# Kernel optimization log

Measured on AMD Instinct MI355X. Metric: run time of the kernel, lower is better.

Reference implementation:

```python
import jax, jax.numpy as jnp
import numpy as np

VOCAB, BLOCK, L, D, H, HD, K = 32000, 4096, 4, 512, 8, 64, 256
EPS = float(jnp.finfo(jnp.float32).eps)


def setup_inputs() -> dict:
    key = jax.random.key(0)
    ks = jax.random.split(key, 16)
    s = 0.02
    inp = {
        "tokens": jax.random.randint(ks[0], (2, 4096), 0, VOCAB),
        "E": jax.random.normal(ks[1], (VOCAB, D), jnp.float32) * s,   # tied token emb / lm_head
        "P": jax.random.normal(ks[2], (BLOCK, D), jnp.float32) * s,   # pos emb
        "Wr": jax.random.normal(ks[3], (L, H, D), jnp.float32) * s,   # router
        "Wq": jax.random.normal(ks[4], (L, D, D), jnp.float32) * s,
        "Wk": jax.random.normal(ks[5], (L, D, D), jnp.float32) * s,
        "Wv": jax.random.normal(ks[6], (L, D, D), jnp.float32) * s,
        "Wo": jax.random.normal(ks[7], (L, D, D), jnp.float32) * s,
        "n1": jnp.ones((L, D), jnp.float32),   # RMSNorm weights
        "n2": jnp.ones((L, D), jnp.float32),
        "W1": jax.random.normal(ks[8], (L, 4 * D, D), jnp.float32) * s,
        "b1": jnp.zeros((L, 4 * D), jnp.float32),
        "W2": jax.random.normal(ks[9], (L, D, 4 * D), jnp.float32) * s,
        "b2": jnp.zeros((L, D), jnp.float32),
    }
    return inp


def rmsnorm(x, w):
    return x * jax.lax.rsqrt(jnp.mean(x * x, axis=-1, keepdims=True) + EPS) * w


def subq_attention(x, Wr, Wq, Wk, Wv, Wo):
    B, T, _ = x.shape
    k_eff = min(K, T)
    # per-head router scores [B, H, T] -> top-k token indices per head
    r = jnp.einsum('btd,hd->bht', x, Wr)
    _, idx = jax.lax.top_k(r, k_eff)                     # [B, H, k]
    q = (x @ Wq.T).reshape(B, T, H, HD).transpose(0, 2, 1, 3)  # [B,H,T,hd]
    k = (x @ Wk.T).reshape(B, T, H, HD).transpose(0, 2, 1, 3)
    v = (x @ Wv.T).reshape(B, T, H, HD).transpose(0, 2, 1, 3)
    ig = idx[..., None]                                   # [B,H,k,1]
    qg = jnp.take_along_axis(q, ig, axis=2)               # [B,H,k,hd]
    kg = jnp.take_along_axis(k, ig, axis=2)
    vg = jnp.take_along_axis(v, ig, axis=2)
    scale = HD ** -0.5
    s = jnp.einsum('bhkd,bhjd->bhkj', qg, kg) * scale     # [B,H,k,k]
    can_attend = idx[:, :, :, None] >= idx[:, :, None, :]  # causal in ORIGINAL positions
    s = jnp.where(can_attend, s, -jnp.inf)
    a = jax.nn.softmax(s, axis=-1)
    og = jnp.einsum('bhkj,bhjd->bhkd', a, vg)             # [B,H,k,hd]
    bb = jnp.arange(B)[:, None, None]
    hh = jnp.arange(H)[None, :, None]
    out = jnp.zeros((B, H, T, HD), x.dtype).at[bb, hh, idx].set(og)  # scatter (indices unique)
    out = out.transpose(0, 2, 1, 3).reshape(B, T, D)
    return out @ Wo.T


def gpt_forward(tokens, E, P, Wr, Wq, Wk, Wv, Wo, n1, n2, W1, b1, W2, b2):
    T = tokens.shape[1]
    x = E[tokens] + P[:T][None, :, :]
    for l in range(L):
        x = x + subq_attention(rmsnorm(x, n1[l]), Wr[l], Wq[l], Wk[l], Wv[l], Wo[l])
        h = rmsnorm(x, n2[l])
        x = x + (jax.nn.silu(h @ W1[l].T + b1[l]) @ W2[l].T + b2[l])
    return x @ E.T  # tied lm_head


def reference(tokens, E, P, Wr, Wq, Wk, Wv, Wo, n1, n2, W1, b1, W2, b2):
    return gpt_forward(tokens, E, P, Wr, Wq, Wk, Wv, Wo, n1, n2, W1, b1, W2, b2)
```

## Files before the change

kernel.cpp:

```cpp
#include <hip/hip_runtime.h>
#include <math.h>

#define BB   2
#define TT   4096
#define DD   512
#define HH   8
#define HDD  64
#define KK   256
#define FF   2048
#define VV   32000
#define LL   4
#define EPSF 1.1920928955078125e-07f

__global__ void embed_k(const int* __restrict__ tok, const float* __restrict__ E,
                        const float* __restrict__ P, float* __restrict__ X) {
    int idx = blockIdx.x * blockDim.x + threadIdx.x;
    int d  = idx & (DD - 1);
    int bt = idx / DD;
    int t  = bt & (TT - 1);
    X[idx] = E[(size_t)tok[bt] * DD + d] + P[t * DD + d];
}

__global__ void rmsnorm_k(const float* __restrict__ X, const float* __restrict__ w,
                          float* __restrict__ Hout) {
    int row = blockIdx.x;
    const float* x = X + (size_t)row * DD;
    int tid = threadIdx.x;
    float v0 = x[tid], v1 = x[tid + 256];
    float ss = v0 * v0 + v1 * v1;
    for (int off = 32; off; off >>= 1) ss += __shfl_down(ss, off);
    __shared__ float red[4];
    __shared__ float sfac;
    if ((tid & 63) == 0) red[tid >> 6] = ss;
    __syncthreads();
    if (tid == 0) {
        float s = red[0] + red[1] + red[2] + red[3];
        sfac = rsqrtf(s * (1.0f / DD) + EPSF);
    }
    __syncthreads();
    float f = sfac;
    Hout[(size_t)row * DD + tid]       = v0 * f * w[tid];
    Hout[(size_t)row * DD + tid + 256] = v1 * f * w[tid + 256];
}

__global__ void router_k(const float* __restrict__ Hb, const float* __restrict__ Wr,
                         float* __restrict__ R) {
    int t = blockIdx.x, h = blockIdx.y, b = blockIdx.z;
    int lane = threadIdx.x;
    const float* x = Hb + ((size_t)(b * TT + t)) * DD;
    const float* w = Wr + h * DD;
    float s = 0.f;
    for (int c = lane; c < DD; c += 64) s += x[c] * w[c];
    for (int off = 32; off; off >>= 1) s += __shfl_down(s, off);
    if (lane == 0) R[((size_t)(b * HH + h)) * TT + t] = s;
}

__global__ void select_k(const float* __restrict__ R, int* __restrict__ IDX) {
    int h = blockIdx.y, b = blockIdx.z;
    const float* r = R + ((size_t)(b * HH + h)) * TT;
    __shared__ float sr[TT];
    for (int i = threadIdx.x; i < TT; i += 256) sr[i] = r[i];
    __syncthreads();
    int t = blockIdx.x * 256 + threadIdx.x;
    float v = sr[t];
    int rank = 0;
    for (int u = 0; u < TT; u++) {
        float ru = sr[u];
        rank += (ru > v) || (ru == v && u < t);
    }
    if (rank < KK) IDX[(b * HH + h) * KK + rank] = t;
}

__global__ void qkv_k(const float* __restrict__ Hb, const int* __restrict__ IDX,
                      const float* __restrict__ Wq, const float* __restrict__ Wk,
                      const float* __restrict__ Wv,
                      float* __restrict__ QG, float* __restrict__ KG, float* __restrict__ VG) {
    int i = blockIdx.x, h = blockIdx.y, b = blockIdx.z;
    int bh = b * HH + h;
    int ti = IDX[bh * KK + i];
    __shared__ float xr[DD];
    int tid = threadIdx.x;
    for (int c = tid; c < DD; c += 192) xr[c] = Hb[((size_t)(b * TT + ti)) * DD + c];
    __syncthreads();
    int which = tid / 64, d = tid & 63;
    const float* W = (which == 0) ? Wq : (which == 1) ? Wk : Wv;
    const float* wrow = W + (size_t)(h * HDD + d) * DD;
    float s = 0.f;
    for (int c = 0; c < DD; c++) s += xr[c] * wrow[c];
    float* Out = (which == 0) ? QG : (which == 1) ? KG : VG;
    Out[((size_t)(bh * KK + i)) * HDD + d] = s;
}

__global__ void attn_k(const float* __restrict__ QG, const float* __restrict__ KG,
                       const float* __restrict__ VG, const int* __restrict__ IDX,
                       float* __restrict__ OG) {
    int i = blockIdx.x, h = blockIdx.y, b = blockIdx.z;
    int bh = b * HH + h;
    const int* idx = IDX + bh * KK;
    __shared__ float q[HDD];
    __shared__ float a[KK];
    __shared__ float red[4];
    int tid = threadIdx.x;
    int ti = idx[i];
    if (tid < HDD) q[tid] = QG[((size_t)(bh * KK + i)) * HDD + tid];
    __syncthreads();
    int j = tid;
    const float* krow = KG + ((size_t)(bh * KK + j)) * HDD;
    float s = 0.f;
    for (int c = 0; c < HDD; c++) s += q[c] * krow[c];
    int tj = idx[j];
    s = (ti >= tj) ? s * 0.125f : -INFINITY;
    float m = s;
    for (int off = 32; off; off >>= 1) m = fmaxf(m, __shfl_down(m, off));
    if ((tid & 63) == 0) red[tid >> 6] = m;
    __syncthreads();
    if (tid == 0) red[0] = fmaxf(fmaxf(red[0], red[1]), fmaxf(red[2], red[3]));
    __syncthreads();
    float mall = red[0];
    float e = expf(s - mall);
    float sum = e;
    for (int off = 32; off; off >>= 1) sum += __shfl_down(sum, off);
    __syncthreads();
    if ((tid & 63) == 0) red[tid >> 6] = sum;
    __syncthreads();
    if (tid == 0) red[0] = red[0] + red[1] + red[2] + red[3];
    __syncthreads();
    float denom = red[0];
    a[tid] = e / denom;
    __syncthreads();
    if (tid < HDD) {
        float o = 0.f;
        for (int jj = 0; jj < KK; jj++) o += a[jj] * VG[((size_t)(bh * KK + jj)) * HDD + tid];
        OG[((size_t)(bh * KK + i)) * HDD + tid] = o;
    }
}

__global__ void oproj_k(const float* __restrict__ OG, const int* __restrict__ IDX,
                        const float* __restrict__ Wo, float* __restrict__ X) {
    int i = blockIdx.x, h = blockIdx.y, b = blockIdx.z;
    int bh = b * HH + h;
    __shared__ float og[HDD];
    int tid = threadIdx.x;
    if (tid < HDD) og[tid] = OG[((size_t)(bh * KK + i)) * HDD + tid];
    __syncthreads();
    int ti = IDX[bh * KK + i];
    const float* wr = Wo + (size_t)tid * DD + h * HDD;
    float s = 0.f;
    for (int c = 0; c < HDD; c++) s += og[c] * wr[c];
    atomicAdd(&X[((size_t)(b * TT + ti)) * DD + tid], s);
}

template <int ACT, int ACC>
__global__ __launch_bounds__(256) void gemm_bt_k(const float* __restrict__ A,
                                                 const float* __restrict__ B,
                                                 const float* __restrict__ bias,
                                                 float* __restrict__ C,
                                                 int M, int N, int Kd) {
    __shared__ float As[16][65];
    __shared__ float Bs[16][65];
    int tx = threadIdx.x, ty = threadIdx.y;
    int tid = ty * 16 + tx;
    int n0 = blockIdx.x * 64, m0 = blockIdx.y * 64;
    float c[4][4] = {};
    int lrow = tid >> 4;
    int lcol = tid & 15;
    for (int k0 = 0; k0 < Kd; k0 += 16) {
#pragma unroll
        for (int i = 0; i < 4; i++) {
            int row = lrow + i * 16;
            As[lcol][row] = A[(size_t)(m0 + row) * Kd + k0 + lcol];
            Bs[lcol][row] = B[(size_t)(n0 + row) * Kd + k0 + lcol];
        }
        __syncthreads();
#pragma unroll
        for (int kk = 0; kk < 16; kk++) {
            float a0 = As[kk][ty * 4 + 0], a1 = As[kk][ty * 4 + 1];
            float a2 = As[kk][ty * 4 + 2], a3 = As[kk][ty * 4 + 3];
            float b0 = Bs[kk][tx * 4 + 0], b1 = Bs[kk][tx * 4 + 1];
            float b2 = Bs[kk][tx * 4 + 2], b3 = Bs[kk][tx * 4 + 3];
            c[0][0] += a0 * b0; c[0][1] += a0 * b1; c[0][2] += a0 * b2; c[0][3] += a0 * b3;
            c[1][0] += a1 * b0; c[1][1] += a1 * b1; c[1][2] += a1 * b2; c[1][3] += a1 * b3;
            c[2][0] += a2 * b0; c[2][1] += a2 * b1; c[2][2] += a2 * b2; c[2][3] += a2 * b3;
            c[3][0] += a3 * b0; c[3][1] += a3 * b1; c[3][2] += a3 * b2; c[3][3] += a3 * b3;
        }
        __syncthreads();
    }
#pragma unroll
    for (int i = 0; i < 4; i++) {
#pragma unroll
        for (int j = 0; j < 4; j++) {
            int m = m0 + ty * 4 + i;
            int n = n0 + tx * 4 + j;
            float v = c[i][j];
            if (bias) v += bias[n];
            if (ACT == 1) v = v / (1.0f + expf(-v));
            size_t o = (size_t)m * N + n;
            if (ACC) C[o] += v; else C[o] = v;
        }
    }
}

extern "C" void kernel_launch(void* const* d_in, const int* in_sizes, int n_in,
                              void* d_out, int out_size, void* d_ws, size_t ws_size,
                              hipStream_t stream) {
    const int*   tok = (const int*)d_in[0];
    const float* E   = (const float*)d_in[1];
    const float* P   = (const float*)d_in[2];
    const float* Wr  = (const float*)d_in[3];
    const float* Wq  = (const float*)d_in[4];
    const float* Wk  = (const float*)d_in[5];
    const float* Wv  = (const float*)d_in[6];
    const float* Wo  = (const float*)d_in[7];
    const float* n1  = (const float*)d_in[8];
    const float* n2  = (const float*)d_in[9];
    const float* W1  = (const float*)d_in[10];
    const float* b1  = (const float*)d_in[11];
    const float* W2  = (const float*)d_in[12];
    const float* b2  = (const float*)d_in[13];
    float* OUT = (float*)d_out;

    float* X = (float*)d_ws;
    float* U   = OUT;
    float* Hb  = U + (size_t)8192 * FF;
    float* R   = Hb + (size_t)8192 * DD;
    float* QG  = R + BB * HH * TT;
    float* KG  = QG + BB * HH * KK * HDD;
    float* VG  = KG + BB * HH * KK * HDD;
    float* OG  = VG + BB * HH * KK * HDD;
    int*   IDX = (int*)(OG + BB * HH * KK * HDD);

    embed_k<<<BB * TT * DD / 256, 256, 0, stream>>>(tok, E, P, X);

    for (int l = 0; l < LL; l++) {
        const float* Wql = Wq + (size_t)l * DD * DD;
        const float* Wkl = Wk + (size_t)l * DD * DD;
        const float* Wvl = Wv + (size_t)l * DD * DD;
        const float* Wol = Wo + (size_t)l * DD * DD;

        rmsnorm_k<<<BB * TT, 256, 0, stream>>>(X, n1 + l * DD, Hb);
        router_k<<<dim3(TT, HH, BB), 64, 0, stream>>>(Hb, Wr + l * HH * DD, R);
        select_k<<<dim3(TT / 256, HH, BB), 256, 0, stream>>>(R, IDX);
        qkv_k<<<dim3(KK, HH, BB), 192, 0, stream>>>(Hb, IDX, Wql, Wkl, Wvl, QG, KG, VG);
        attn_k<<<dim3(KK, HH, BB), 256, 0, stream>>>(QG, KG, VG, IDX, OG);
        oproj_k<<<dim3(KK, HH, BB), 512, 0, stream>>>(OG, IDX, Wol, X);

        rmsnorm_k<<<BB * TT, 256, 0, stream>>>(X, n2 + l * DD, Hb);
        gemm_bt_k<1, 0><<<dim3(FF / 64, BB * TT / 64), dim3(16, 16), 0, stream>>>(
            Hb, W1 + (size_t)l * FF * DD, b1 + l * FF, U, BB * TT, FF, DD);
        gemm_bt_k<0, 1><<<dim3(DD / 64, BB * TT / 64), dim3(16, 16), 0, stream>>>(
            U, W2 + (size_t)l * DD * FF, b2 + l * DD, X, BB * TT, DD, FF);
    }

    gemm_bt_k<0, 0><<<dim3(VV / 64, BB * TT / 64), dim3(16, 16), 0, stream>>>(
        X, E, nullptr, OUT, BB * TT, VV, DD);
}
```

Measured before the change: 10.67 ms.

## Use larger register-tiled double-buffered GEMM with float4 loads and stores

Rewrites the FP32 GEMM to compute 128x128 (or 128x64) output tiles per 256-thread block, with 8x8 or 8x4 accumulators per thread instead of 4x4. Global loads and shared-memory reads use float4, and shared memory is double-buffered with register prefetch of the next K-slice, so only one barrier is needed per step. The goal is higher arithmetic intensity and latency hiding in the FFN and lm_head GEMMs. In exchange it uses more registers per thread, which may lower occupancy.

```diff
diff --git a/kernel.cpp b/kernel.cpp
--- a/kernel.cpp
+++ b/kernel.cpp
@@ -150,52 +150,111 @@
     atomicAdd(&X[((size_t)(b * TT + ti)) * DD + tid], s);
 }
 
-template <int ACT, int ACC>
+template <int ACT, int ACC, int TN>
 __global__ __launch_bounds__(256) void gemm_bt_k(const float* __restrict__ A,
                                                  const float* __restrict__ B,
                                                  const float* __restrict__ bias,
                                                  float* __restrict__ C,
                                                  int M, int N, int Kd) {
-    __shared__ float As[16][65];
-    __shared__ float Bs[16][65];
-    int tx = threadIdx.x, ty = threadIdx.y;
-    int tid = ty * 16 + tx;
-    int n0 = blockIdx.x * 64, m0 = blockIdx.y * 64;
-    float c[4][4] = {};
-    int lrow = tid >> 4;
-    int lcol = tid & 15;
-    for (int k0 = 0; k0 < Kd; k0 += 16) {
-#pragma unroll
-        for (int i = 0; i < 4; i++) {
-            int row = lrow + i * 16;
-            As[lcol][row] = A[(size_t)(m0 + row) * Kd + k0 + lcol];
-            Bs[lcol][row] = B[(size_t)(n0 + row) * Kd + k0 + lcol];
+    constexpr int NB = TN / 64;
+    constexpr int BPAD = (TN == 128) ? 132 : 68;
+    __shared__ __attribute__((aligned(16))) float As[2][16][132];
+    __shared__ __attribute__((aligned(16))) float Bs[2][16][BPAD];
+    const int tid = threadIdx.x;
+    const int tx = tid & 15, ty = tid >> 4;
+    const int n0 = blockIdx.x * TN;
+    const int m0 = blockIdx.y * 128;
+    const int lr = tid >> 2;
+    const int lc = (tid & 3) * 4;
+    const float* Ap = A + (size_t)(m0 + lr) * Kd + lc;
+    const float* Bp = B + (size_t)(n0 + lr) * Kd + lc;
+    const size_t str64 = (size_t)64 * Kd;
+
+    float4 ra[2], rb[NB];
+    ra[0] = *(const float4*)Ap;
+    ra[1] = *(const float4*)(Ap + str64);
+    rb[0] = *(const float4*)Bp;
+    if constexpr (NB == 2) rb[1] = *(const float4*)(Bp + str64);
+#pragma unroll
+    for (int j = 0; j < 4; j++) {
+        As[0][lc + j][lr]      = ((const float*)&ra[0])[j];
+        As[0][lc + j][lr + 64] = ((const float*)&ra[1])[j];
+        Bs[0][lc + j][lr]      = ((const float*)&rb[0])[j];
+        if constexpr (NB == 2) Bs[0][lc + j][lr + 64] = ((const float*)&rb[1])[j];
+    }
+
+    float acc[2][NB][4][4] = {};
+    const int nsteps = Kd >> 4;
+    int cur = 0;
+    for (int t = 0; t < nsteps; t++) {
+        if (t + 1 < nsteps) {
+            const float* Ap2 = Ap + (t + 1) * 16;
+            const float* Bp2 = Bp + (t + 1) * 16;
+            ra[0] = *(const float4*)Ap2;
+            ra[1] = *(const float4*)(Ap2 + str64);
+            rb[0] = *(const float4*)Bp2;
+            if constexpr (NB == 2) rb[1] = *(const float4*)(Bp2 + str64);
         }
         __syncthreads();
 #pragma unroll
         for (int kk = 0; kk < 16; kk++) {
-            float a0 = As[kk][ty * 4 + 0], a1 = As[kk][ty * 4 + 1];
-            float a2 = As[kk][ty * 4 + 2], a3 = As[kk][ty * 4 + 3];
-            float b0 = Bs[kk][tx * 4 + 0], b1 = Bs[kk][tx * 4 + 1];
-            float b2 = Bs[kk][tx * 4 + 2], b3 = Bs[kk][tx * 4 + 3];
-            c[0][0] += a0 * b0; c[0][1] += a0 * b1; c[0][2] += a0 * b2; c[0][3] += a0 * b3;
-            c[1][0] += a1 * b0; c[1][1] += a1 * b1; c[1][2] += a1 * b2; c[1][3] += a1 * b3;
-            c[2][0] += a2 * b0; c[2][1] += a2 * b1; c[2][2] += a2 * b2; c[2][3] += a2 * b3;
-            c[3][0] += a3 * b0; c[3][1] += a3 * b1; c[3][2] += a3 * b2; c[3][3] += a3 * b3;
+            float4 av0 = *(const float4*)&As[cur][kk][ty * 4];
+            float4 av1 = *(const float4*)&As[cur][kk][64 + ty * 4];
+            float4 bv[NB];
+            bv[0] = *(const float4*)&Bs[cur][kk][tx * 4];
+            if constexpr (NB == 2) bv[1] = *(const float4*)&Bs[cur][kk][64 + tx * 4];
+            const float* af0 = (const float*)&av0;
+            const float* af1 = (const float*)&av1;
+#pragma unroll
+            for (int i = 0; i < 4; i++) {
+                float a0 = af0[i], a1 = af1[i];
+#pragma unroll
+                for (int hn = 0; hn < NB; hn++) {
+                    const float* bf = (const float*)&bv[hn];
+#pragma unroll
+                    for (int j = 0; j < 4; j++) {
+                        acc[0][hn][i][j] += a0 * bf[j];
+                        acc[1][hn][i][j] += a1 * bf[j];
+                    }
+                }
+            }
         }
-        __syncthreads();
-    }
-#pragma unroll
-    for (int i = 0; i < 4; i++) {
-#pragma unroll
-        for (int j = 0; j < 4; j++) {
-            int m = m0 + ty * 4 + i;
-            int n = n0 + tx * 4 + j;
-            float v = c[i][j];
-            if (bias) v += bias[n];
-            if (ACT == 1) v = v / (1.0f + expf(-v));
-            size_t o = (size_t)m * N + n;
-            if (ACC) C[o] += v; else C[o] = v;
+        if (t + 1 < nsteps) {
+            int nxt = cur ^ 1;
+#pragma unroll
+            for (int j = 0; j < 4; j++) {
+                As[nxt][lc + j][lr]      = ((const float*)&ra[0])[j];
+                As[nxt][lc + j][lr + 64] = ((const float*)&ra[1])[j];
+                Bs[nxt][lc + j][lr]      = ((const float*)&rb[0])[j];
+                if constexpr (NB == 2) Bs[nxt][lc + j][lr + 64] = ((const float*)&rb[1])[j];
+            }
+            cur = nxt;
+        }
+    }
+#pragma unroll
+    for (int hm = 0; hm < 2; hm++) {
+#pragma unroll
+        for (int i = 0; i < 4; i++) {
+            int m = m0 + hm * 64 + ty * 4 + i;
+#pragma unroll
+            for (int hn = 0; hn < NB; hn++) {
+                int n = n0 + hn * 64 + tx * 4;
+                float4 v;
+                float* vf = (float*)&v;
+#pragma unroll
+                for (int j = 0; j < 4; j++) {
+                    float x = acc[hm][hn][i][j];
+                    if (bias) x += bias[n + j];
+                    if (ACT == 1) x = x / (1.0f + expf(-x));
+                    vf[j] = x;
+                }
+                float* Cp = C + (size_t)m * N + n;
+                if constexpr (ACC) {
+                    float4 old = *(const float4*)Cp;
+                    v.x += old.x; v.y += old.y; v.z += old.z; v.w += old.w;
+                }
+                *(float4*)Cp = v;
+            }
         }
     }
 }
@@ -245,12 +304,12 @@
         oproj_k<<<dim3(KK, HH, BB), 512, 0, stream>>>(OG, IDX, Wol, X);
 
         rmsnorm_k<<<BB * TT, 256, 0, stream>>>(X, n2 + l * DD, Hb);
-        gemm_bt_k<1, 0><<<dim3(FF / 64, BB * TT / 64), dim3(16, 16), 0, stream>>>(
+        gemm_bt_k<1, 0, 128><<<dim3(FF / 128, BB * TT / 128), 256, 0, stream>>>(
             Hb, W1 + (size_t)l * FF * DD, b1 + l * FF, U, BB * TT, FF, DD);
-        gemm_bt_k<0, 1><<<dim3(DD / 64, BB * TT / 64), dim3(16, 16), 0, stream>>>(
+        gemm_bt_k<0, 1, 64><<<dim3(DD / 64, BB * TT / 128), 256, 0, stream>>>(
             U, W2 + (size_t)l * DD * FF, b2 + l * DD, X, BB * TT, DD, FF);
     }
 
-    gemm_bt_k<0, 0><<<dim3(VV / 64, BB * TT / 64), dim3(16, 16), 0, stream>>>(
+    gemm_bt_k<0, 0, 128><<<dim3(VV / 128, BB * TT / 128), 256, 0, stream>>>(
         X, E, nullptr, OUT, BB * TT, VV, DD);
 }
```

Result: faster. 9.330 ms (-12.5%).
